# Kernel tuning notes

Hardware: AMD Instinct MI355X
Metric: run time of the kernel (lower is better)

## Reference

```python
import jax, jax.numpy as jnp
import numpy as np

N, K, D, H = 100000, 16, 128, 4
HD = D // H
EPS = 1e-5


def layer_norm(x, g, b):
    mu = jnp.mean(x, axis=-1, keepdims=True)
    var = jnp.mean(jnp.square(x - mu), axis=-1, keepdims=True)
    return (x - mu) * jax.lax.rsqrt(var + EPS) * g + b


def setup_inputs() -> dict:
    key = jax.random.key(0)
    ks = jax.random.split(key, 8)
    s = 0.02
    x = jax.random.normal(ks[0], (N, D), jnp.float32)
    attention_samples = jax.random.randint(ks[1], (N, K), 0, N)
    in_proj_w = jax.random.normal(ks[2], (3 * D, D), jnp.float32) * s
    in_proj_b = jnp.zeros((3 * D,), jnp.float32)
    out_w = jax.random.normal(ks[3], (D, D), jnp.float32) * s
    out_b = jnp.zeros((D,), jnp.float32)
    ffn_w1 = jax.random.normal(ks[4], (4 * D, D), jnp.float32) * s
    ffn_b1 = jnp.zeros((4 * D,), jnp.float32)
    ffn_w2 = jax.random.normal(ks[5], (D, 4 * D), jnp.float32) * s
    ffn_b2 = jnp.zeros((D,), jnp.float32)
    ln1_g = jnp.ones((D,), jnp.float32)
    ln1_b = jnp.zeros((D,), jnp.float32)
    ln2_g = jnp.ones((D,), jnp.float32)
    ln2_b = jnp.zeros((D,), jnp.float32)
    return dict(x=x, attention_samples=attention_samples, in_proj_w=in_proj_w,
                in_proj_b=in_proj_b, out_w=out_w, out_b=out_b,
                ffn_w1=ffn_w1, ffn_b1=ffn_b1, ffn_w2=ffn_w2, ffn_b2=ffn_b2,
                ln1_g=ln1_g, ln1_b=ln1_b, ln2_g=ln2_g, ln2_b=ln2_b)


def reference(x, attention_samples, in_proj_w, in_proj_b, out_w, out_b,
              ffn_w1, ffn_b1, ffn_w2, ffn_b2, ln1_g, ln1_b, ln2_g, ln2_b):
    n = x.shape[0]
    k = attention_samples.shape[1]
    wq, wk, wv = in_proj_w[:D], in_proj_w[D:2 * D], in_proj_w[2 * D:]
    bq, bk, bv = in_proj_b[:D], in_proj_b[D:2 * D], in_proj_b[2 * D:]
    # Project first (one [N,D] GEMM each), then gather the projections.
    # Mathematically identical to torch's gather-then-project (projection is per-row linear).
    q = x @ wq.T + bq                      # [N, D]
    kx = x @ wk.T + bk                     # [N, D]
    vx = x @ wv.T + bv                     # [N, D]
    k_s = kx[attention_samples]            # [N, K, D]
    v_s = vx[attention_samples]            # [N, K, D]
    qh = q.reshape(n, H, HD)               # [N, H, HD]
    kh = k_s.reshape(n, k, H, HD)          # [N, K, H, HD]
    vh = v_s.reshape(n, k, H, HD)
    scores = jnp.einsum('nhd,nkhd->nhk', qh, kh) / np.sqrt(HD).astype(np.float32)
    w = jax.nn.softmax(scores, axis=-1)    # [N, H, K]
    attn = jnp.einsum('nhk,nkhd->nhd', w, vh).reshape(n, D)
    attn = attn @ out_w.T + out_b          # out_proj
    x = layer_norm(x + attn, ln1_g, ln1_b)
    h = jax.nn.relu(x @ ffn_w1.T + ffn_b1)
    x = layer_norm(x + h @ ffn_w2.T + ffn_b2, ln2_g, ln2_b)
    return x
```

## Files before the change

### kernel.cpp

```cpp
#include <hip/hip_runtime.h>
#include <hip/hip_bf16.h>
#include <hip/hip_fp8.h>

#define NTOK 100000
#define EPS 1e-5f

using frag  = __attribute__((ext_vector_type(8))) short;
using f32x4 = __attribute__((ext_vector_type(4))) float;
typedef __hip_bfloat16 bf16;
typedef unsigned short ushort_t;

__device__ inline float bits2f(unsigned int u) { union { unsigned int i; float f; } x; x.i = u; return x.f; }
__device__ inline void bfu_unpack(unsigned int u, float& lo, float& hi) {
  lo = bits2f(u << 16);
  hi = bits2f(u & 0xffff0000u);
}

__device__ inline float4 fp8x4_to_f4(unsigned int u) {
  __hip_fp8_e4m3 a, b, c, d;
  a.__x = u & 0xff; b.__x = (u >> 8) & 0xff; c.__x = (u >> 16) & 0xff; d.__x = (u >> 24) & 0xff;
  return make_float4((float)a, (float)b, (float)c, (float)d);
}
__device__ inline unsigned char f_to_fp8(float f) { __hip_fp8_e4m3 t(f); return t.__x; }

#define GL_LDS16(gsrc, ldst)                                                  \
  __builtin_amdgcn_global_load_lds(                                           \
      (const __attribute__((address_space(1))) void*)(gsrc),                  \
      (__attribute__((address_space(3))) void*)(ldst), 16, 0, 0)

__global__ __launch_bounds__(256) void cvt_x_kernel(const float* __restrict__ in,
                                                    bf16* __restrict__ out) {
  const int e = (blockIdx.x * 256 + threadIdx.x) * 4;
  float4 v = *(const float4*)&in[e];
  bf16 o[4] = {__float2bfloat16(v.x), __float2bfloat16(v.y),
               __float2bfloat16(v.z), __float2bfloat16(v.w)};
  *(ulong1*)&out[e] = *(ulong1*)o;
}

__global__ __launch_bounds__(256) void cvt_w_kernel(
    const float* __restrict__ w0, const float* __restrict__ w1,
    const float* __restrict__ w2, const float* __restrict__ w3,
    bf16* __restrict__ out) {
  const int e = (blockIdx.x * 256 + threadIdx.x) * 4;
  const float* src;
  int off;
  if (e < 49152)       { src = w0; off = 0; }
  else if (e < 65536)  { src = w1; off = 49152; }
  else if (e < 131072) { src = w2; off = 65536; }
  else                 { src = w3; off = 131072; }
  float4 v = *(const float4*)&src[e - off];
  bf16 o[4] = {__float2bfloat16(v.x), __float2bfloat16(v.y),
               __float2bfloat16(v.z), __float2bfloat16(v.w)};
  *(ulong1*)&out[e] = *(ulong1*)o;
}

__device__ __forceinline__ void stage_B(const bf16* __restrict__ Wslab, int KTOT,
                                        int c, ushort_t* Bs, int tid) {
#pragma unroll
  for (int r = 0; r < 8; ++r) {
    const int g = r * 256 + tid, row = g >> 4, u = g & 15;
    GL_LDS16(Wslab + (size_t)row * KTOT + (size_t)c * 128 + (u ^ (row & 15)) * 8,
             Bs + g * 8);
  }
}

__device__ __forceinline__ void gemm_body128(
    const bf16* __restrict__ A, const bf16* __restrict__ Wslab,
    int row0, int M, ushort_t* Bs, f32x4 (&acc)[2][8]) {
  const int tid = threadIdx.x;
  const int lane = tid & 63;
  const int lr = lane & 15, kg = lane >> 4;

  int r0 = row0 + lr;      if (r0 > M - 1) r0 = M - 1;
  int r1 = row0 + 16 + lr; if (r1 > M - 1) r1 = M - 1;
  const bf16* a0 = A + (size_t)r0 * 128 + kg * 8;
  const bf16* a1 = A + (size_t)r1 * 128 + kg * 8;

  frag a[2][4];
#pragma unroll
  for (int kc = 0; kc < 4; ++kc) {
    a[0][kc] = *(const frag*)(a0 + kc * 32);
    a[1][kc] = *(const frag*)(a1 + kc * 32);
  }
  stage_B(Wslab, 128, 0, Bs, tid);
  __syncthreads();

#pragma unroll
  for (int kc = 0; kc < 4; ++kc) {
    const int uoff = ((kc * 4 + kg) ^ lr) * 8;
#pragma unroll
    for (int j = 0; j < 8; ++j) {
      frag b = *(const frag*)&Bs[(lr + 16 * j) * 128 + uoff];
      acc[0][j] = __builtin_amdgcn_mfma_f32_16x16x32_bf16(a[0][kc], b, acc[0][j], 0, 0, 0);
      acc[1][j] = __builtin_amdgcn_mfma_f32_16x16x32_bf16(a[1][kc], b, acc[1][j], 0, 0, 0);
    }
  }
}

__global__ __launch_bounds__(256, 4) void k_qkv(
    const bf16* __restrict__ A, const bf16* __restrict__ W,
    const float* __restrict__ bias, bf16* __restrict__ qout,
    unsigned char* __restrict__ kout, unsigned char* __restrict__ vout, int M) {
  __shared__ ushort_t Bs[16384];
  const int lane = threadIdx.x & 63;
  const int wid = threadIdx.x >> 6;
  const int row0 = blockIdx.x * 128 + wid * 32;
  const int cbase = blockIdx.y * 128;
  const int lr = lane & 15, kg = lane >> 4;

  f32x4 acc[2][8] = {};
  gemm_body128(A, W + (size_t)cbase * 128, row0, M, Bs, acc);

  float bs[8];
#pragma unroll
  for (int j = 0; j < 8; ++j) bs[j] = bias[cbase + lr + 16 * j];
  const int y = blockIdx.y;
  unsigned char* f8dst = (y == 1) ? kout : vout;
#pragma unroll
  for (int i = 0; i < 2; ++i)
#pragma unroll
    for (int r = 0; r < 4; ++r) {
      const int row = row0 + 16 * i + 4 * kg + r;
      if (row >= M) continue;
      if (y == 0) {
        bf16* orow = qout + (size_t)row * 128 + lr;
#pragma unroll
        for (int j = 0; j < 8; ++j) orow[16 * j] = __float2bfloat16(acc[i][j][r] + bs[j]);
      } else {
        unsigned char* orow = f8dst + (size_t)row * 128 + lr;
#pragma unroll
        for (int j = 0; j < 8; ++j) orow[16 * j] = f_to_fp8(acc[i][j][r] + bs[j]);
      }
    }
}

__global__ __launch_bounds__(256, 4) void k_ffn1(
    const bf16* __restrict__ A, const bf16* __restrict__ W,
    const float* __restrict__ bias, bf16* __restrict__ out, int M) {
  __shared__ ushort_t Bs[16384];
  const int lane = threadIdx.x & 63;
  const int wid = threadIdx.x >> 6;
  const int row0 = blockIdx.x * 128 + wid * 32;
  const int cbase = blockIdx.y * 128;
  const int lr = lane & 15, kg = lane >> 4;

  f32x4 acc[2][8] = {};
  gemm_body128(A, W + (size_t)cbase * 128, row0, M, Bs, acc);

  float bs[8];
#pragma unroll
  for (int j = 0; j < 8; ++j) bs[j] = bias[cbase + lr + 16 * j];
#pragma unroll
  for (int i = 0; i < 2; ++i)
#pragma unroll
    for (int r = 0; r < 4; ++r) {
      const int row = row0 + 16 * i + 4 * kg + r;
      if (row >= M) continue;
      bf16* orow = out + (size_t)row * 512 + cbase + lr;
#pragma unroll
      for (int j = 0; j < 8; ++j)
        orow[16 * j] = __float2bfloat16(fmaxf(acc[i][j][r] + bs[j], 0.f));
    }
}

__global__ __launch_bounds__(256, 4) void k_outproj_ln(
    const bf16* __restrict__ A, const bf16* __restrict__ W,
    const float* __restrict__ bias, const bf16* __restrict__ resid,
    const float* __restrict__ g, const float* __restrict__ b,
    bf16* __restrict__ out, int M) {
  __shared__ ushort_t Bs[16384];
  const int lane = threadIdx.x & 63;
  const int wid = threadIdx.x >> 6;
  const int row0 = blockIdx.x * 128 + wid * 32;
  const int lr = lane & 15, kg = lane >> 4;

  f32x4 acc[2][8] = {};
  gemm_body128(A, W, row0, M, Bs, acc);

  float bs[8], gs[8], bbs[8];
#pragma unroll
  for (int j = 0; j < 8; ++j) {
    const int c = lr + 16 * j;
    bs[j] = bias[c]; gs[j] = g[c]; bbs[j] = b[c];
  }
#pragma unroll
  for (int i = 0; i < 2; ++i)
#pragma unroll
    for (int r = 0; r < 4; ++r) {
      const int row = row0 + 16 * i + 4 * kg + r;
      const int rr = (row > M - 1) ? (M - 1) : row;
      const bf16* rrow = resid + (size_t)rr * 128 + lr;
      float v[8], psum = 0.f, psq = 0.f;
#pragma unroll
      for (int j = 0; j < 8; ++j) {
        v[j] = acc[i][j][r] + bs[j] + __bfloat162float(rrow[16 * j]);
        psum += v[j];
        psq += v[j] * v[j];
      }
#pragma unroll
      for (int off = 1; off < 16; off <<= 1) {
        psum += __shfl_xor(psum, off);
        psq += __shfl_xor(psq, off);
      }
      const float mean = psum * (1.f / 128.f);
      const float var = psq * (1.f / 128.f) - mean * mean;
      const float rstd = rsqrtf(var + EPS);
      if (row < M) {
        bf16* orow = out + (size_t)row * 128 + lr;
#pragma unroll
        for (int j = 0; j < 8; ++j)
          orow[16 * j] = __float2bfloat16((v[j] - mean) * rstd * gs[j] + bbs[j]);
      }
    }
}

__global__ __launch_bounds__(256, 2) void k_ffn2_ln(
    const bf16* __restrict__ A,
    const bf16* __restrict__ W,
    const float* __restrict__ bias, const bf16* __restrict__ resid,
    const float* __restrict__ g, const float* __restrict__ b,
    float* __restrict__ out, int M) {
  __shared__ ushort_t Bs0[16384];
  __shared__ ushort_t Bs1[16384];
  const int tid = threadIdx.x;
  const int lane = tid & 63;
  const int wid = tid >> 6;
  const int row0 = blockIdx.x * 128 + wid * 32;
  const int lr = lane & 15, kg = lane >> 4;

  int r0 = row0 + lr;      if (r0 > M - 1) r0 = M - 1;
  int r1 = row0 + 16 + lr; if (r1 > M - 1) r1 = M - 1;
  const bf16* a0 = A + (size_t)r0 * 512 + kg * 8;
  const bf16* a1 = A + (size_t)r1 * 512 + kg * 8;

  f32x4 acc[2][8] = {};
  frag aC0[4], aC1[4], aN0[4], aN1[4];

#define LDA(d0, d1, c)                                            \
  { _Pragma("unroll") for (int kc = 0; kc < 4; ++kc) {            \
      d0[kc] = *(const frag*)(a0 + (c) * 128 + kc * 32);          \
      d1[kc] = *(const frag*)(a1 + (c) * 128 + kc * 32); } }
#define STEP(B, s0, s1)                                           \
  { _Pragma("unroll") for (int kc = 0; kc < 4; ++kc) {            \
      const int uo = ((kc * 4 + kg) ^ lr) * 8;                    \
      _Pragma("unroll") for (int j = 0; j < 8; ++j) {             \
        frag bb = *(const frag*)&B[(lr + 16 * j) * 128 + uo];     \
        acc[0][j] = __builtin_amdgcn_mfma_f32_16x16x32_bf16(s0[kc], bb, acc[0][j], 0, 0, 0); \
        acc[1][j] = __builtin_amdgcn_mfma_f32_16x16x32_bf16(s1[kc], bb, acc[1][j], 0, 0, 0); } } }

  LDA(aC0, aC1, 0);
  stage_B(W, 512, 0, Bs0, tid);
  __syncthreads();

  LDA(aN0, aN1, 1);
  stage_B(W, 512, 1, Bs1, tid);
  STEP(Bs0, aC0, aC1);
  __syncthreads();

  LDA(aC0, aC1, 2);
  stage_B(W, 512, 2, Bs0, tid);
  STEP(Bs1, aN0, aN1);
  __syncthreads();

  LDA(aN0, aN1, 3);
  stage_B(W, 512, 3, Bs1, tid);
  STEP(Bs0, aC0, aC1);
  __syncthreads();

  STEP(Bs1, aN0, aN1);
#undef LDA
#undef STEP

  float bs[8], gs[8], bbs[8];
#pragma unroll
  for (int j = 0; j < 8; ++j) {
    const int c = lr + 16 * j;
    bs[j] = bias[c]; gs[j] = g[c]; bbs[j] = b[c];
  }
#pragma unroll
  for (int i = 0; i < 2; ++i)
#pragma unroll
    for (int r = 0; r < 4; ++r) {
      const int row = row0 + 16 * i + 4 * kg + r;
      const int rr = (row > M - 1) ? (M - 1) : row;
      const bf16* rrow = resid + (size_t)rr * 128 + lr;
      float v[8], psum = 0.f, psq = 0.f;
#pragma unroll
      for (int j = 0; j < 8; ++j) {
        v[j] = acc[i][j][r] + bs[j] + __bfloat162float(rrow[16 * j]);
        psum += v[j];
        psq += v[j] * v[j];
      }
#pragma unroll
      for (int off = 1; off < 16; off <<= 1) {
        psum += __shfl_xor(psum, off);
        psq += __shfl_xor(psq, off);
      }
      const float mean = psum * (1.f / 128.f);
      const float var = psq * (1.f / 128.f) - mean * mean;
      const float rstd = rsqrtf(var + EPS);
      if (row < M) {
        float* orow = out + (size_t)row * 128 + lr;
#pragma unroll
        for (int j = 0; j < 8; ++j)
          orow[16 * j] = (v[j] - mean) * rstd * gs[j] + bbs[j];
      }
    }
}

__global__ __launch_bounds__(256) void attn_kernel(
    const bf16* __restrict__ qb, const unsigned char* __restrict__ kf8,
    const unsigned char* __restrict__ vf8, const int* __restrict__ samples,
    bf16* __restrict__ attn) {
  const int lane = threadIdx.x & 63;
  const int wid = threadIdx.x >> 6;
  const int tok = blockIdx.x * 4 + wid;
  if (tok >= NTOK) return;
  const int qt = lane >> 4;
  const int lr = lane & 15;

  const float scale = 0.17677669529663687f;
  float q8[8];
  {
    uint4 qu = *(const uint4*)&qb[(size_t)tok * 128 + 8 * lr];
    bfu_unpack(qu.x, q8[0], q8[1]);
    bfu_unpack(qu.y, q8[2], q8[3]);
    bfu_unpack(qu.z, q8[4], q8[5]);
    bfu_unpack(qu.w, q8[6], q8[7]);
#pragma unroll
    for (int d = 0; d < 8; ++d) q8[d] *= scale;
  }

  const int myidx = samples[tok * 16 + lr];
  int kidx[4];
#pragma unroll
  for (int jj = 0; jj < 4; ++jj) kidx[jj] = __shfl(myidx, 4 * jj + qt, 16);

  float s[4];
#pragma unroll
  for (int jj = 0; jj < 4; ++jj) {
    uint2 ku = *(const uint2*)&kf8[(size_t)kidx[jj] * 128 + 8 * lr];
    float4 k0 = fp8x4_to_f4(ku.x), k1 = fp8x4_to_f4(ku.y);
    float p = q8[0] * k0.x + q8[1] * k0.y + q8[2] * k0.z + q8[3] * k0.w +
              q8[4] * k1.x + q8[5] * k1.y + q8[6] * k1.z + q8[7] * k1.w;
    p += __shfl_xor(p, 1);
    p += __shfl_xor(p, 2);
    s[jj] = p;
  }

  float m = fmaxf(fmaxf(s[0], s[1]), fmaxf(s[2], s[3]));
  m = fmaxf(m, __shfl_xor(m, 16));
  m = fmaxf(m, __shfl_xor(m, 32));
  float sum = 0.f;
#pragma unroll
  for (int jj = 0; jj < 4; ++jj) {
    s[jj] = __expf(s[jj] - m);
    sum += s[jj];
  }
  sum += __shfl_xor(sum, 16);
  sum += __shfl_xor(sum, 32);
  const float inv = 1.f / sum;

  float a8[8] = {};
#pragma unroll
  for (int jj = 0; jj < 4; ++jj) {
    uint2 vu = *(const uint2*)&vf8[(size_t)kidx[jj] * 128 + 8 * lr];
    float4 v0 = fp8x4_to_f4(vu.x), v1 = fp8x4_to_f4(vu.y);
    const float wj = s[jj] * inv;
    a8[0] += wj * v0.x; a8[1] += wj * v0.y; a8[2] += wj * v0.z; a8[3] += wj * v0.w;
    a8[4] += wj * v1.x; a8[5] += wj * v1.y; a8[6] += wj * v1.z; a8[7] += wj * v1.w;
  }
#pragma unroll
  for (int d = 0; d < 8; ++d) {
    a8[d] += __shfl_xor(a8[d], 16);
    a8[d] += __shfl_xor(a8[d], 32);
  }

  if (qt == 0) {
    uint4 o;
    o.x = (unsigned)__bfloat16_as_ushort(__float2bfloat16(a8[0])) |
          ((unsigned)__bfloat16_as_ushort(__float2bfloat16(a8[1])) << 16);
    o.y = (unsigned)__bfloat16_as_ushort(__float2bfloat16(a8[2])) |
          ((unsigned)__bfloat16_as_ushort(__float2bfloat16(a8[3])) << 16);
    o.z = (unsigned)__bfloat16_as_ushort(__float2bfloat16(a8[4])) |
          ((unsigned)__bfloat16_as_ushort(__float2bfloat16(a8[5])) << 16);
    o.w = (unsigned)__bfloat16_as_ushort(__float2bfloat16(a8[6])) |
          ((unsigned)__bfloat16_as_ushort(__float2bfloat16(a8[7])) << 16);
    *(uint4*)&attn[(size_t)tok * 128 + 8 * lr] = o;
  }
}

extern "C" void kernel_launch(void* const* d_in, const int* in_sizes, int n_in,
                              void* d_out, int out_size, void* d_ws, size_t ws_size,
                              hipStream_t stream) {
  const float* x      = (const float*)d_in[0];
  const int* samples  = (const int*)d_in[1];
  const float* in_w   = (const float*)d_in[2];
  const float* in_b   = (const float*)d_in[3];
  const float* out_w  = (const float*)d_in[4];
  const float* out_b  = (const float*)d_in[5];
  const float* ffn_w1 = (const float*)d_in[6];
  const float* ffn_b1 = (const float*)d_in[7];
  const float* ffn_w2 = (const float*)d_in[8];
  const float* ffn_b2 = (const float*)d_in[9];
  const float* ln1_g  = (const float*)d_in[10];
  const float* ln1_b  = (const float*)d_in[11];
  const float* ln2_g  = (const float*)d_in[12];
  const float* ln2_b  = (const float*)d_in[13];
  float* out = (float*)d_out;

  char* ws = (char*)d_ws;
  bf16* xb   = (bf16*)(ws);
  bf16* qb   = (bf16*)(ws + 25600000);
  unsigned char* kf8 = (unsigned char*)(ws + 51200000);
  unsigned char* vf8 = (unsigned char*)(ws + 64000000);
  bf16* attn = (bf16*)(ws + 76800000);
  bf16* h    = (bf16*)(ws);
  bf16* x1b  = (bf16*)(ws + 102400000);
  bf16* wb   = (bf16*)(ws + 128000000);
  bf16* in_wb   = wb;
  bf16* out_wb  = wb + 49152;
  bf16* ffn_w1b = wb + 65536;
  bf16* ffn_w2b = wb + 131072;

  const int M = NTOK;
  dim3 blk(256);
  const int gm = (M + 127) / 128;

  cvt_x_kernel<<<dim3(12500), blk, 0, stream>>>(x, xb);
  cvt_w_kernel<<<dim3(192), blk, 0, stream>>>(in_w, out_w, ffn_w1, ffn_w2, wb);
  k_qkv<<<dim3(gm, 3), blk, 0, stream>>>(xb, in_wb, in_b, qb, kf8, vf8, M);
  attn_kernel<<<dim3((M + 3) / 4), blk, 0, stream>>>(qb, kf8, vf8, samples, attn);
  k_outproj_ln<<<dim3(gm), blk, 0, stream>>>(attn, out_wb, out_b, xb, ln1_g, ln1_b, x1b, M);
  k_ffn1<<<dim3(gm, 4), blk, 0, stream>>>(x1b, ffn_w1b, ffn_b1, h, M);
  k_ffn2_ln<<<dim3(gm), blk, 0, stream>>>(h, ffn_w2b, ffn_b2, x1b, ln2_g, ln2_b, out, M);
}
```

Measured before the change: 196.9 us.

## Loop over output column tiles inside QKV and FFN1 blocks to reuse A fragments

The QKV and FFN1 GEMMs no longer launch one block per 128-column tile (grid y=3/4). Each block now loads its A rows into registers once and loops over all column tiles, restaging the weight slab into LDS each iteration. This removes redundant global reads of the activation rows, in exchange for fewer blocks, serialized weight staging with extra barriers, and less parallelism per launch. The ffn2 kernel is refactored to use a shared mfma helper.

```diff
diff --git a/kernel.cpp b/kernel.cpp
--- a/kernel.cpp
+++ b/kernel.cpp
@@ -55,36 +55,16 @@
 }
 
 __device__ __forceinline__ void stage_B(const bf16* __restrict__ Wslab, int KTOT,
-                                        int c, ushort_t* Bs, int tid) {
+                                        ushort_t* Bs, int tid) {
 #pragma unroll
   for (int r = 0; r < 8; ++r) {
     const int g = r * 256 + tid, row = g >> 4, u = g & 15;
-    GL_LDS16(Wslab + (size_t)row * KTOT + (size_t)c * 128 + (u ^ (row & 15)) * 8,
-             Bs + g * 8);
-  }
-}
-
-__device__ __forceinline__ void gemm_body128(
-    const bf16* __restrict__ A, const bf16* __restrict__ Wslab,
-    int row0, int M, ushort_t* Bs, f32x4 (&acc)[2][8]) {
-  const int tid = threadIdx.x;
-  const int lane = tid & 63;
-  const int lr = lane & 15, kg = lane >> 4;
-
-  int r0 = row0 + lr;      if (r0 > M - 1) r0 = M - 1;
-  int r1 = row0 + 16 + lr; if (r1 > M - 1) r1 = M - 1;
-  const bf16* a0 = A + (size_t)r0 * 128 + kg * 8;
-  const bf16* a1 = A + (size_t)r1 * 128 + kg * 8;
-
-  frag a[2][4];
-#pragma unroll
-  for (int kc = 0; kc < 4; ++kc) {
-    a[0][kc] = *(const frag*)(a0 + kc * 32);
-    a[1][kc] = *(const frag*)(a1 + kc * 32);
-  }
-  stage_B(Wslab, 128, 0, Bs, tid);
-  __syncthreads();
-
+    GL_LDS16(Wslab + (size_t)row * KTOT + (u ^ (row & 15)) * 8, Bs + g * 8);
+  }
+}
+
+__device__ __forceinline__ void mfma_step(const frag (&a)[2][4], ushort_t* Bs,
+                                          int lr, int kg, f32x4 (&acc)[2][8]) {
 #pragma unroll
   for (int kc = 0; kc < 4; ++kc) {
     const int uoff = ((kc * 4 + kg) ^ lr) * 8;
@@ -102,65 +82,96 @@
     const float* __restrict__ bias, bf16* __restrict__ qout,
     unsigned char* __restrict__ kout, unsigned char* __restrict__ vout, int M) {
   __shared__ ushort_t Bs[16384];
-  const int lane = threadIdx.x & 63;
-  const int wid = threadIdx.x >> 6;
+  const int tid = threadIdx.x;
+  const int lane = tid & 63;
+  const int wid = tid >> 6;
   const int row0 = blockIdx.x * 128 + wid * 32;
-  const int cbase = blockIdx.y * 128;
   const int lr = lane & 15, kg = lane >> 4;
 
-  f32x4 acc[2][8] = {};
-  gemm_body128(A, W + (size_t)cbase * 128, row0, M, Bs, acc);
-
-  float bs[8];
-#pragma unroll
-  for (int j = 0; j < 8; ++j) bs[j] = bias[cbase + lr + 16 * j];
-  const int y = blockIdx.y;
-  unsigned char* f8dst = (y == 1) ? kout : vout;
-#pragma unroll
-  for (int i = 0; i < 2; ++i)
-#pragma unroll
-    for (int r = 0; r < 4; ++r) {
-      const int row = row0 + 16 * i + 4 * kg + r;
-      if (row >= M) continue;
-      if (y == 0) {
-        bf16* orow = qout + (size_t)row * 128 + lr;
-#pragma unroll
-        for (int j = 0; j < 8; ++j) orow[16 * j] = __float2bfloat16(acc[i][j][r] + bs[j]);
-      } else {
-        unsigned char* orow = f8dst + (size_t)row * 128 + lr;
-#pragma unroll
-        for (int j = 0; j < 8; ++j) orow[16 * j] = f_to_fp8(acc[i][j][r] + bs[j]);
-      }
-    }
+  int r0 = row0 + lr;      if (r0 > M - 1) r0 = M - 1;
+  int r1 = row0 + 16 + lr; if (r1 > M - 1) r1 = M - 1;
+  frag a[2][4];
+#pragma unroll
+  for (int kc = 0; kc < 4; ++kc) {
+    a[0][kc] = *(const frag*)(A + (size_t)r0 * 128 + kg * 8 + kc * 32);
+    a[1][kc] = *(const frag*)(A + (size_t)r1 * 128 + kg * 8 + kc * 32);
+  }
+
+#pragma unroll
+  for (int cc = 0; cc < 3; ++cc) {
+    if (cc > 0) __syncthreads();
+    stage_B(W + (size_t)cc * 128 * 128, 128, Bs, tid);
+    __syncthreads();
+
+    f32x4 acc[2][8] = {};
+    mfma_step(a, Bs, lr, kg, acc);
+
+    float bs[8];
+#pragma unroll
+    for (int j = 0; j < 8; ++j) bs[j] = bias[cc * 128 + lr + 16 * j];
+    unsigned char* f8dst = (cc == 1) ? kout : vout;
+#pragma unroll
+    for (int i = 0; i < 2; ++i)
+#pragma unroll
+      for (int r = 0; r < 4; ++r) {
+        const int row = row0 + 16 * i + 4 * kg + r;
+        if (row >= M) continue;
+        if (cc == 0) {
+          bf16* orow = qout + (size_t)row * 128 + lr;
+#pragma unroll
+          for (int j = 0; j < 8; ++j) orow[16 * j] = __float2bfloat16(acc[i][j][r] + bs[j]);
+        } else {
+          unsigned char* orow = f8dst + (size_t)row * 128 + lr;
+#pragma unroll
+          for (int j = 0; j < 8; ++j) orow[16 * j] = f_to_fp8(acc[i][j][r] + bs[j]);
+        }
+      }
+  }
 }
 
 __global__ __launch_bounds__(256, 4) void k_ffn1(
     const bf16* __restrict__ A, const bf16* __restrict__ W,
     const float* __restrict__ bias, bf16* __restrict__ out, int M) {
   __shared__ ushort_t Bs[16384];
-  const int lane = threadIdx.x & 63;
-  const int wid = threadIdx.x >> 6;
+  const int tid = threadIdx.x;
+  const int lane = tid & 63;
+  const int wid = tid >> 6;
   const int row0 = blockIdx.x * 128 + wid * 32;
-  const int cbase = blockIdx.y * 128;
   const int lr = lane & 15, kg = lane >> 4;
 
-  f32x4 acc[2][8] = {};
-  gemm_body128(A, W + (size_t)cbase * 128, row0, M, Bs, acc);
-
-  float bs[8];
-#pragma unroll
-  for (int j = 0; j < 8; ++j) bs[j] = bias[cbase + lr + 16 * j];
-#pragma unroll
-  for (int i = 0; i < 2; ++i)
-#pragma unroll
-    for (int r = 0; r < 4; ++r) {
-      const int row = row0 + 16 * i + 4 * kg + r;
-      if (row >= M) continue;
-      bf16* orow = out + (size_t)row * 512 + cbase + lr;
-#pragma unroll
-      for (int j = 0; j < 8; ++j)
-        orow[16 * j] = __float2bfloat16(fmaxf(acc[i][j][r] + bs[j], 0.f));
-    }
+  int r0 = row0 + lr;      if (r0 > M - 1) r0 = M - 1;
+  int r1 = row0 + 16 + lr; if (r1 > M - 1) r1 = M - 1;
+  frag a[2][4];
+#pragma unroll
+  for (int kc = 0; kc < 4; ++kc) {
+    a[0][kc] = *(const frag*)(A + (size_t)r0 * 128 + kg * 8 + kc * 32);
+    a[1][kc] = *(const frag*)(A + (size_t)r1 * 128 + kg * 8 + kc * 32);
+  }
+
+#pragma unroll
+  for (int cc = 0; cc < 4; ++cc) {
+    if (cc > 0) __syncthreads();
+    stage_B(W + (size_t)cc * 128 * 128, 128, Bs, tid);
+    __syncthreads();
+
+    f32x4 acc[2][8] = {};
+    mfma_step(a, Bs, lr, kg, acc);
+
+    float bs[8];
+#pragma unroll
+    for (int j = 0; j < 8; ++j) bs[j] = bias[cc * 128 + lr + 16 * j];
+#pragma unroll
+    for (int i = 0; i < 2; ++i)
+#pragma unroll
+      for (int r = 0; r < 4; ++r) {
+        const int row = row0 + 16 * i + 4 * kg + r;
+        if (row >= M) continue;
+        bf16* orow = out + (size_t)row * 512 + cc * 128 + lr;
+#pragma unroll
+        for (int j = 0; j < 8; ++j)
+          orow[16 * j] = __float2bfloat16(fmaxf(acc[i][j][r] + bs[j], 0.f));
+      }
+  }
 }
 
 __global__ __launch_bounds__(256, 4) void k_outproj_ln(
@@ -169,13 +180,25 @@
     const float* __restrict__ g, const float* __restrict__ b,
     bf16* __restrict__ out, int M) {
   __shared__ ushort_t Bs[16384];
-  const int lane = threadIdx.x & 63;
-  const int wid = threadIdx.x >> 6;
+  const int tid = threadIdx.x;
+  const int lane = tid & 63;
+  const int wid = tid >> 6;
   const int row0 = blockIdx.x * 128 + wid * 32;
   const int lr = lane & 15, kg = lane >> 4;
 
+  int r0 = row0 + lr;      if (r0 > M - 1) r0 = M - 1;
+  int r1 = row0 + 16 + lr; if (r1 > M - 1) r1 = M - 1;
+  frag a[2][4];
+#pragma unroll
+  for (int kc = 0; kc < 4; ++kc) {
+    a[0][kc] = *(const frag*)(A + (size_t)r0 * 128 + kg * 8 + kc * 32);
+    a[1][kc] = *(const frag*)(A + (size_t)r1 * 128 + kg * 8 + kc * 32);
+  }
+  stage_B(W, 128, Bs, tid);
+  __syncthreads();
+
   f32x4 acc[2][8] = {};
-  gemm_body128(A, W, row0, M, Bs, acc);
+  mfma_step(a, Bs, lr, kg, acc);
 
   float bs[8], gs[8], bbs[8];
 #pragma unroll
@@ -234,42 +257,39 @@
   const bf16* a1 = A + (size_t)r1 * 512 + kg * 8;
 
   f32x4 acc[2][8] = {};
-  frag aC0[4], aC1[4], aN0[4], aN1[4];
-
-#define LDA(d0, d1, c)                                            \
+  frag aC[2][4], aN[2][4];
+
+#define LDA(d, c)                                                 \
   { _Pragma("unroll") for (int kc = 0; kc < 4; ++kc) {            \
-      d0[kc] = *(const frag*)(a0 + (c) * 128 + kc * 32);          \
-      d1[kc] = *(const frag*)(a1 + (c) * 128 + kc * 32); } }
-#define STEP(B, s0, s1)                                           \
-  { _Pragma("unroll") for (int kc = 0; kc < 4; ++kc) {            \
-      const int uo = ((kc * 4 + kg) ^ lr) * 8;                    \
-      _Pragma("unroll") for (int j = 0; j < 8; ++j) {             \
-        frag bb = *(const frag*)&B[(lr + 16 * j) * 128 + uo];     \
-        acc[0][j] = __builtin_amdgcn_mfma_f32_16x16x32_bf16(s0[kc], bb, acc[0][j], 0, 0, 0); \
-        acc[1][j] = __builtin_amdgcn_mfma_f32_16x16x32_bf16(s1[kc], bb, acc[1][j], 0, 0, 0); } } }
-
-  LDA(aC0, aC1, 0);
-  stage_B(W, 512, 0, Bs0, tid);
+      d[0][kc] = *(const frag*)(a0 + (c) * 128 + kc * 32);        \
+      d[1][kc] = *(const frag*)(a1 + (c) * 128 + kc * 32); } }
+#define STAGE(Bsx, c)                                             \
+  { _Pragma("unroll") for (int r = 0; r < 8; ++r) {               \
+      const int gg = r * 256 + tid, row = gg >> 4, u = gg & 15;   \
+      GL_LDS16(W + (size_t)row * 512 + (c) * 128 + (u ^ (row & 15)) * 8, Bsx + gg * 8); } }
+
+  LDA(aC, 0);
+  STAGE(Bs0, 0);
   __syncthreads();
 
-  LDA(aN0, aN1, 1);
-  stage_B(W, 512, 1, Bs1, tid);
-  STEP(Bs0, aC0, aC1);
+  LDA(aN, 1);
+  STAGE(Bs1, 1);
+  mfma_step(aC, Bs0, lr, kg, acc);
   __syncthreads();
 
-  LDA(aC0, aC1, 2);
-  stage_B(W, 512, 2, Bs0, tid);
-  STEP(Bs1, aN0, aN1);
+  LDA(aC, 2);
+  STAGE(Bs0, 2);
+  mfma_step(aN, Bs1, lr, kg, acc);
   __syncthreads();
 
-  LDA(aN0, aN1, 3);
-  stage_B(W, 512, 3, Bs1, tid);
-  STEP(Bs0, aC0, aC1);
+  LDA(aN, 3);
+  STAGE(Bs1, 3);
+  mfma_step(aC, Bs0, lr, kg, acc);
   __syncthreads();
 
-  STEP(Bs1, aN0, aN1);
+  mfma_step(aN, Bs1, lr, kg, acc);
 #undef LDA
-#undef STEP
+#undef STAGE
 
   float bs[8], gs[8], bbs[8];
 #pragma unroll
@@ -429,9 +449,9 @@
 
   cvt_x_kernel<<<dim3(12500), blk, 0, stream>>>(x, xb);
   cvt_w_kernel<<<dim3(192), blk, 0, stream>>>(in_w, out_w, ffn_w1, ffn_w2, wb);
-  k_qkv<<<dim3(gm, 3), blk, 0, stream>>>(xb, in_wb, in_b, qb, kf8, vf8, M);
+  k_qkv<<<dim3(gm), blk, 0, stream>>>(xb, in_wb, in_b, qb, kf8, vf8, M);
   attn_kernel<<<dim3((M + 3) / 4), blk, 0, stream>>>(qb, kf8, vf8, samples, attn);
   k_outproj_ln<<<dim3(gm), blk, 0, stream>>>(attn, out_wb, out_b, xb, ln1_g, ln1_b, x1b, M);
-  k_ffn1<<<dim3(gm, 4), blk, 0, stream>>>(x1b, ffn_w1b, ffn_b1, h, M);
+  k_ffn1<<<dim3(gm), blk, 0, stream>>>(x1b, ffn_w1b, ffn_b1, h, M);
   k_ffn2_ln<<<dim3(gm), blk, 0, stream>>>(h, ffn_w2b, ffn_b2, x1b, ln2_g, ln2_b, out, M);
 }
```

Result: slower. 274.9 us (+39.6%).
